# Performance work log

Hardware: AMD Instinct MI355X
Metric: run time of the kernel (lower is better)

The kernel has to match this reference:

```python
import jax, jax.numpy as jnp
import numpy as np

SEQ, BATCH, HID = 4096, 32, 512


def setup_inputs() -> dict:
    key = jax.random.key(0)
    ks = jax.random.split(key, 7)
    s = 1.0 / np.sqrt(HID)
    return {
        "x0": jax.random.normal(ks[0], (SEQ, BATCH, 1), dtype=jnp.float32),
        "W_ih": jax.random.uniform(ks[1], (4 * HID, 1), jnp.float32, -s, s),
        "W_hh": jax.random.uniform(ks[2], (4 * HID, HID), jnp.float32, -s, s),
        "b_ih": jax.random.uniform(ks[3], (4 * HID,), jnp.float32, -s, s),
        "b_hh": jax.random.uniform(ks[4], (4 * HID,), jnp.float32, -s, s),
        "W_lin": jax.random.uniform(ks[5], (1, HID), jnp.float32, -s, s),
        "b_lin": jax.random.uniform(ks[6], (1,), jnp.float32, -s, s),
    }


def _lstm(x0, W_ih, W_hh, b_ih, b_hh):
    # x0: (T, B, 1). Precompute input contribution to gates for all steps.
    x_proj = jnp.einsum("tbi,gi->tbg", x0, W_ih) + (b_ih + b_hh)  # (T, B, 4H)
    T, B, _ = x_proj.shape
    H = W_hh.shape[1]
    h0 = jnp.zeros((B, H), x0.dtype)
    c0 = jnp.zeros((B, H), x0.dtype)

    def step(carry, xp):
        h, c = carry
        gates = xp + h @ W_hh.T  # (B, 4H)
        i, f, g, o = jnp.split(gates, 4, axis=-1)  # torch gate order i,f,g,o
        i = jax.nn.sigmoid(i)
        f = jax.nn.sigmoid(f)
        g = jnp.tanh(g)
        o = jax.nn.sigmoid(o)
        c = f * c + i * g
        h = o * jnp.tanh(c)
        return (h, c), h

    _, hs = jax.lax.scan(step, (h0, c0), x_proj)  # hs: (T, B, H)
    return hs


def reference(x0, W_ih, W_hh, b_ih, b_hh, W_lin, b_lin):
    hs = _lstm(x0, W_ih, W_hh, b_ih, b_hh)            # (T, B, H)
    y = jnp.einsum("tbh,oh->tbo", hs, W_lin) + b_lin  # (T, B, 1)
    return y + x0                                      # residual add
```

## Files before the change

### kernel.cpp

```cpp
#include <hip/hip_runtime.h>
#include <stdint.h>

#define T_STEPS 4096
#define BATCH 32
#define HID 512
#define GROUPS 8
#define BLK_THREADS 512
#define NBLOCKS 256
#define SLOT_DW (BATCH * GROUPS * 64)

typedef _Float16 h2_t __attribute__((ext_vector_type(2)));
typedef uint32_t u32x8 __attribute__((ext_vector_type(8)));

__device__ inline uint32_t pack_h2(float a, float b) {
  h2_t v;
  v.x = (_Float16)a;
  v.y = (_Float16)b;
  return __builtin_bit_cast(uint32_t, v);
}

__device__ inline float fdot2(uint32_t a, uint32_t b, float c) {
  return __builtin_amdgcn_fdot2(__builtin_bit_cast(h2_t, a),
                                __builtin_bit_cast(h2_t, b), c, false);
}

__device__ inline uint64_t uni64(const void* p) {
  uint32_t lo = __builtin_amdgcn_readfirstlane((uint32_t)(uintptr_t)p);
  uint32_t hi = __builtin_amdgcn_readfirstlane((uint32_t)((uintptr_t)p >> 32));
  return ((uint64_t)hi << 32) | lo;
}

__device__ inline void kinv() {
  asm volatile("s_dcache_inv" ::: "memory");
}

__device__ inline void sload_rec(uint64_t p, u32x8* d0, u32x8* d1,
                                 u32x8* d2, u32x8* d3,
                                 uint32_t* t0, uint32_t* t1,
                                 uint32_t* t2, uint32_t* t3) {
  asm volatile("s_load_dwordx8 %0, %8, 0x0\n\t"
               "s_load_dword %4, %8, 0x20\n\t"
               "s_load_dwordx8 %1, %8, 0x40\n\t"
               "s_load_dword %5, %8, 0x60\n\t"
               "s_load_dwordx8 %2, %8, 0x80\n\t"
               "s_load_dword %6, %8, 0xa0\n\t"
               "s_load_dwordx8 %3, %8, 0xc0\n\t"
               "s_load_dword %7, %8, 0xe0\n\t"
               "s_waitcnt lgkmcnt(0)"
               : "=&s"(*d0), "=&s"(*d1), "=&s"(*d2), "=&s"(*d3),
                 "=&s"(*t0), "=&s"(*t1), "=&s"(*t2), "=&s"(*t3)
               : "s"(p) : "memory");
}

__device__ inline float sigf(float x) { return 1.0f / (1.0f + __expf(-x)); }
__device__ inline float tanh_fast(float x) {
  float a = fabsf(x);
  float e = __expf(-2.0f * a);
  float r = (1.0f - e) / (1.0f + e);
  return copysignf(r, x);
}

__global__ __launch_bounds__(BLK_THREADS)
void lstm_w8(const float* __restrict__ x0,
             const float* __restrict__ W_ih,
             const float* __restrict__ W_hh,
             const float* __restrict__ b_ih,
             const float* __restrict__ b_hh,
             const float* __restrict__ W_lin,
             const float* __restrict__ b_lin,
             float* __restrict__ y,
             uint32_t* __restrict__ h_ex,
             int* __restrict__ claim)
{
  __shared__ float x0_lds[T_STEPS];
  __shared__ float ylds[T_STEPS];
  __shared__ float gacc[2][256];
  __shared__ int arrive[2];
  __shared__ int s_bg;

  const int tid = threadIdx.x;

  if (tid == 0) {
    uint32_t xcc;
    asm volatile("s_getreg_b32 %0, hwreg(HW_REG_XCC_ID)" : "=s"(xcc));
    xcc &= 7;
    int slot = atomicAdd(claim + xcc * 16, 1);
    s_bg = (slot < 32) ? (int)(((4 * xcc + (slot >> 3)) << 3) | (slot & 7))
                       : -1;
  }
  __syncthreads();
  if (s_bg < 0) return;
  const int b  = s_bg >> 3;
  const int g  = s_bg & 7;
  const int u0 = g * 64;
  const int wv = tid >> 6;
  const int cs = wv;
  const int l  = tid & 63;

  uint32_t w[4][32];
#pragma unroll
  for (int a = 0; a < 4; ++a) {
    const int R = a * HID + u0 + l;
    const float2* p = (const float2*)(W_hh + (size_t)R * HID + 64 * cs);
#pragma unroll
    for (int k = 0; k < 32; ++k) {
      float2 q = p[k];
      w[a][k] = pack_h2(q.x, q.y);
    }
  }
  for (int i = tid; i < T_STEPS; i += BLK_THREADS) {
    x0_lds[i] = x0[i * BATCH + b];
    ylds[i] = 0.f;
  }
  if (tid < 256) { gacc[0][tid] = 0.f; gacc[1][tid] = 0.f; }
  if (tid < 2) arrive[tid] = 0;

  float c_state = 0.f;
  float wih_[4] = {0.f, 0.f, 0.f, 0.f}, bs_[4] = {0.f, 0.f, 0.f, 0.f};
  float wlin_u = 0.f, blin = 0.f;
  if (tid < 64) {
#pragma unroll
    for (int j = 0; j < 4; ++j) {
      int R = j * HID + u0 + tid;
      wih_[j] = W_ih[R];
      bs_[j] = b_ih[R] + b_hh[R];
    }
    wlin_u = W_lin[u0 + tid];
    blin = b_lin[0];
  }

  uint32_t* hb = h_ex + (size_t)b * (GROUPS * 64);
  const uint64_t dpu[2] = { uni64(hb + 64 * cs),
                            uni64(hb + SLOT_DW + 64 * cs) };
  uint32_t* pub01[2] = { hb + 64 * g, hb + SLOT_DW + 64 * g };

  __syncthreads();

  int dead = 0;
  for (int t = 0; t < T_STEPS; ++t) {
    const int sl = t & 1, ns = sl ^ 1;

    u32x8 D0, D1, D2, D3;
    uint32_t tg0, tg1, tg2, tg3;
    {
      const uint32_t want = (uint32_t)t;
      int guard = 0;
      for (;;) {
        kinv();
        sload_rec(dpu[sl], &D0, &D1, &D2, &D3, &tg0, &tg1, &tg2, &tg3);
        if ((tg0 == want) & (tg1 == want) &
            (tg2 == want) & (tg3 == want)) break;
        if (dead || ++guard > (1 << 14)) { dead = 1; break; }
      }
    }

    __builtin_amdgcn_s_setprio(1);
    float ae0 = 0.f, ao0 = 0.f, ae1 = 0.f, ao1 = 0.f;
    float ae2 = 0.f, ao2 = 0.f, ae3 = 0.f, ao3 = 0.f;
#pragma unroll
    for (int k = 0; k < 8; k += 2) {
      ae0 = fdot2(w[0][k], D0[k], ae0);      ao0 = fdot2(w[0][k + 1], D0[k + 1], ao0);
      ae1 = fdot2(w[1][k], D0[k], ae1);      ao1 = fdot2(w[1][k + 1], D0[k + 1], ao1);
      ae2 = fdot2(w[2][k], D0[k], ae2);      ao2 = fdot2(w[2][k + 1], D0[k + 1], ao2);
      ae3 = fdot2(w[3][k], D0[k], ae3);      ao3 = fdot2(w[3][k + 1], D0[k + 1], ao3);
      ae0 = fdot2(w[0][8 + k], D1[k], ae0);  ao0 = fdot2(w[0][9 + k], D1[k + 1], ao0);
      ae1 = fdot2(w[1][8 + k], D1[k], ae1);  ao1 = fdot2(w[1][9 + k], D1[k + 1], ao1);
      ae2 = fdot2(w[2][8 + k], D1[k], ae2);  ao2 = fdot2(w[2][9 + k], D1[k + 1], ao2);
      ae3 = fdot2(w[3][8 + k], D1[k], ae3);  ao3 = fdot2(w[3][9 + k], D1[k + 1], ao3);
      ae0 = fdot2(w[0][16 + k], D2[k], ae0); ao0 = fdot2(w[0][17 + k], D2[k + 1], ao0);
      ae1 = fdot2(w[1][16 + k], D2[k], ae1); ao1 = fdot2(w[1][17 + k], D2[k + 1], ao1);
      ae2 = fdot2(w[2][16 + k], D2[k], ae2); ao2 = fdot2(w[2][17 + k], D2[k + 1], ao2);
      ae3 = fdot2(w[3][16 + k], D2[k], ae3); ao3 = fdot2(w[3][17 + k], D2[k + 1], ao3);
      ae0 = fdot2(w[0][24 + k], D3[k], ae0); ao0 = fdot2(w[0][25 + k], D3[k + 1], ao0);
      ae1 = fdot2(w[1][24 + k], D3[k], ae1); ao1 = fdot2(w[1][25 + k], D3[k + 1], ao1);
      ae2 = fdot2(w[2][24 + k], D3[k], ae2); ao2 = fdot2(w[2][25 + k], D3[k + 1], ao2);
      ae3 = fdot2(w[3][24 + k], D3[k], ae3); ao3 = fdot2(w[3][25 + k], D3[k + 1], ao3);
    }
    atomicAdd(&gacc[sl][l],       ae0 + ao0);
    atomicAdd(&gacc[sl][64 + l],  ae1 + ao1);
    atomicAdd(&gacc[sl][128 + l], ae2 + ao2);
    atomicAdd(&gacc[sl][192 + l], ae3 + ao3);
    asm volatile("" ::: "memory");
    if (l == 0) atomicAdd(&arrive[sl], 1);
    __builtin_amdgcn_s_setprio(0);

    if (tid < 64) {
      {
        int guard = 0;
        while (((volatile int*)arrive)[sl] < 8) {
          if (++guard > (1 << 20)) break;
        }
      }
      asm volatile("" ::: "memory");
      __builtin_amdgcn_s_setprio(1);
      arrive[sl] = 0;

      const float xv = x0_lds[t];
      float gi = gacc[sl][tid]       + xv * wih_[0] + bs_[0];
      float gf = gacc[sl][tid + 64]  + xv * wih_[1] + bs_[1];
      float gg = gacc[sl][tid + 128] + xv * wih_[2] + bs_[2];
      float go = gacc[sl][tid + 192] + xv * wih_[3] + bs_[3];
      float si = sigf(gi), sf = sigf(gf), tg_ = tanh_fast(gg), so = sigf(go);
      c_state = sf * c_state + si * tg_;
      float h = so * tanh_fast(c_state);

      float hn = __shfl_down(h, 1, 64);
      uint32_t val = 0;
      int doff = 0;
      bool act = false;
      if ((tid & 1) == 0) {
        int j = tid >> 1;
        val = pack_h2(h, hn);
        doff = ((j >> 3) << 4) + (j & 7);
        act = true;
      } else if (tid < 8) {
        int L = (tid - 1) >> 1;
        val = (uint32_t)(t + 1);
        doff = (L << 4) + 8;
        act = true;
      }
      if (act) pub01[ns][doff] = val;

      gacc[sl][tid] = 0.f;
      gacc[sl][tid + 64] = 0.f;
      gacc[sl][tid + 128] = 0.f;
      gacc[sl][tid + 192] = 0.f;

      float p = wlin_u * h;
#pragma unroll
      for (int m = 32; m >= 1; m >>= 1) p += __shfl_xor(p, m, 64);
      if (tid == 0) ylds[t] = p;
      __builtin_amdgcn_s_setprio(0);
    }
  }

  __syncthreads();
  for (int i = tid; i < T_STEPS; i += BLK_THREADS) {
    float val = ylds[i];
    if (g == 0) val += blin + x0_lds[i];
    unsafeAtomicAdd(&y[i * BATCH + b], val);
  }
}

extern "C" void kernel_launch(void* const* d_in, const int* in_sizes, int n_in,
                              void* d_out, int out_size, void* d_ws, size_t ws_size,
                              hipStream_t stream) {
  const float* x0    = (const float*)d_in[0];
  const float* W_ih  = (const float*)d_in[1];
  const float* W_hh  = (const float*)d_in[2];
  const float* b_ih  = (const float*)d_in[3];
  const float* b_hh  = (const float*)d_in[4];
  const float* W_lin = (const float*)d_in[5];
  const float* b_lin = (const float*)d_in[6];
  float* y = (float*)d_out;

  uint32_t* h_ex = (uint32_t*)d_ws;
  int* claim     = (int*)(h_ex + 2 * SLOT_DW);
  const size_t init_bytes = (size_t)2 * SLOT_DW * sizeof(uint32_t)
                            + 8 * 16 * sizeof(int);

  (void)hipMemsetAsync(d_ws, 0, init_bytes, stream);
  (void)hipMemsetAsync(d_out, 0, (size_t)out_size * sizeof(float), stream);

  hipLaunchKernelGGL(lstm_w8, dim3(NBLOCKS), dim3(BLK_THREADS), 0, stream,
                     x0, W_ih, W_hh, b_ih, b_hh, W_lin, b_lin, y, h_ex, claim);
}
```

Baseline: 13.97 ms.

## Let wave 0 consume its own hidden slice from LDS and skip global polling

Each block's wave 0 now handles the column slice that this block produces itself (cs rotated by the group index). It reads that slice from a small LDS ring buffer instead of polling global memory, so the wave no longer waits on a global round trip for its own data. Wave 0 also takes over the gate nonlinearity, and the output projection for the previous step is deferred and computed from the fp16-rounded h stored in LDS. This moves work off the critical path between steps. The cost is that y is now computed from fp16-rounded h, which adds a small precision loss, and wave 0 carries more work per step.

```diff
diff --git a/kernel.cpp b/kernel.cpp
--- a/kernel.cpp
+++ b/kernel.cpp
@@ -10,6 +10,7 @@
 #define SLOT_DW (BATCH * GROUPS * 64)
 
 typedef _Float16 h2_t __attribute__((ext_vector_type(2)));
+typedef uint32_t u32x4 __attribute__((ext_vector_type(4)));
 typedef uint32_t u32x8 __attribute__((ext_vector_type(8)));
 
 __device__ inline uint32_t pack_h2(float a, float b) {
@@ -61,20 +62,21 @@
 }
 
 __global__ __launch_bounds__(BLK_THREADS)
-void lstm_w8(const float* __restrict__ x0,
-             const float* __restrict__ W_ih,
-             const float* __restrict__ W_hh,
-             const float* __restrict__ b_ih,
-             const float* __restrict__ b_hh,
-             const float* __restrict__ W_lin,
-             const float* __restrict__ b_lin,
-             float* __restrict__ y,
-             uint32_t* __restrict__ h_ex,
-             int* __restrict__ claim)
+void lstm_w8t(const float* __restrict__ x0,
+              const float* __restrict__ W_ih,
+              const float* __restrict__ W_hh,
+              const float* __restrict__ b_ih,
+              const float* __restrict__ b_hh,
+              const float* __restrict__ W_lin,
+              const float* __restrict__ b_lin,
+              float* __restrict__ y,
+              uint32_t* __restrict__ h_ex,
+              int* __restrict__ claim)
 {
   __shared__ float x0_lds[T_STEPS];
   __shared__ float ylds[T_STEPS];
   __shared__ float gacc[2][256];
+  __shared__ __align__(16) uint32_t h_self[4][32];
   __shared__ int arrive[2];
   __shared__ int s_bg;
 
@@ -94,7 +96,7 @@
   const int g  = s_bg & 7;
   const int u0 = g * 64;
   const int wv = tid >> 6;
-  const int cs = wv;
+  const int cs = (g + wv) & 7;
   const int l  = tid & 63;
 
   uint32_t w[4][32];
@@ -113,11 +115,13 @@
     ylds[i] = 0.f;
   }
   if (tid < 256) { gacc[0][tid] = 0.f; gacc[1][tid] = 0.f; }
+  if (tid < 128) ((uint32_t*)h_self)[tid] = 0;
   if (tid < 2) arrive[tid] = 0;
 
   float c_state = 0.f;
   float wih_[4] = {0.f, 0.f, 0.f, 0.f}, bs_[4] = {0.f, 0.f, 0.f, 0.f};
-  float wlin_u = 0.f, blin = 0.f;
+  float wlin_u = 0.f;
+  const float blin = b_lin[0];
   if (tid < 64) {
 #pragma unroll
     for (int j = 0; j < 4; ++j) {
@@ -126,7 +130,6 @@
       bs_[j] = b_ih[R] + b_hh[R];
     }
     wlin_u = W_lin[u0 + tid];
-    blin = b_lin[0];
   }
 
   uint32_t* hb = h_ex + (size_t)b * (GROUPS * 64);
@@ -140,98 +143,136 @@
   for (int t = 0; t < T_STEPS; ++t) {
     const int sl = t & 1, ns = sl ^ 1;
 
-    u32x8 D0, D1, D2, D3;
-    uint32_t tg0, tg1, tg2, tg3;
+    if (wv != 0) {
+      u32x8 D0, D1, D2, D3;
+      uint32_t tg0, tg1, tg2, tg3;
+      {
+        const uint32_t want = (uint32_t)t;
+        int guard = 0;
+        for (;;) {
+          kinv();
+          sload_rec(dpu[sl], &D0, &D1, &D2, &D3, &tg0, &tg1, &tg2, &tg3);
+          if ((tg0 == want) & (tg1 == want) &
+              (tg2 == want) & (tg3 == want)) break;
+          if (dead || ++guard > (1 << 14)) { dead = 1; break; }
+        }
+      }
+      __builtin_amdgcn_s_setprio(1);
+      float ae0 = 0.f, ao0 = 0.f, ae1 = 0.f, ao1 = 0.f;
+      float ae2 = 0.f, ao2 = 0.f, ae3 = 0.f, ao3 = 0.f;
+#pragma unroll
+      for (int k = 0; k < 8; k += 2) {
+        ae0 = fdot2(w[0][k], D0[k], ae0);      ao0 = fdot2(w[0][k + 1], D0[k + 1], ao0);
+        ae1 = fdot2(w[1][k], D0[k], ae1);      ao1 = fdot2(w[1][k + 1], D0[k + 1], ao1);
+        ae2 = fdot2(w[2][k], D0[k], ae2);      ao2 = fdot2(w[2][k + 1], D0[k + 1], ao2);
+        ae3 = fdot2(w[3][k], D0[k], ae3);      ao3 = fdot2(w[3][k + 1], D0[k + 1], ao3);
+        ae0 = fdot2(w[0][8 + k], D1[k], ae0);  ao0 = fdot2(w[0][9 + k], D1[k + 1], ao0);
+        ae1 = fdot2(w[1][8 + k], D1[k], ae1);  ao1 = fdot2(w[1][9 + k], D1[k + 1], ao1);
+        ae2 = fdot2(w[2][8 + k], D1[k], ae2);  ao2 = fdot2(w[2][9 + k], D1[k + 1], ao2);
+        ae3 = fdot2(w[3][8 + k], D1[k], ae3);  ao3 = fdot2(w[3][9 + k], D1[k + 1], ao3);
+        ae0 = fdot2(w[0][16 + k], D2[k], ae0); ao0 = fdot2(w[0][17 + k], D2[k + 1], ao0);
+        ae1 = fdot2(w[1][16 + k], D2[k], ae1); ao1 = fdot2(w[1][17 + k], D2[k + 1], ao1);
+        ae2 = fdot2(w[2][16 + k], D2[k], ae2); ao2 = fdot2(w[2][17 + k], D2[k + 1], ao2);
+        ae3 = fdot2(w[3][16 + k], D2[k], ae3); ao3 = fdot2(w[3][17 + k], D2[k + 1], ao3);
+        ae0 = fdot2(w[0][24 + k], D3[k], ae0); ao0 = fdot2(w[0][25 + k], D3[k + 1], ao0);
+        ae1 = fdot2(w[1][24 + k], D3[k], ae1); ao1 = fdot2(w[1][25 + k], D3[k + 1], ao1);
+        ae2 = fdot2(w[2][24 + k], D3[k], ae2); ao2 = fdot2(w[2][25 + k], D3[k + 1], ao2);
+        ae3 = fdot2(w[3][24 + k], D3[k], ae3); ao3 = fdot2(w[3][25 + k], D3[k + 1], ao3);
+      }
+      atomicAdd(&gacc[sl][l],       ae0 + ao0);
+      atomicAdd(&gacc[sl][64 + l],  ae1 + ao1);
+      atomicAdd(&gacc[sl][128 + l], ae2 + ao2);
+      atomicAdd(&gacc[sl][192 + l], ae3 + ao3);
+      asm volatile("" ::: "memory");
+      if (l == 0) atomicAdd(&arrive[sl], 1);
+      __builtin_amdgcn_s_setprio(0);
+      continue;
+    }
+
+    __builtin_amdgcn_s_setprio(1);
     {
-      const uint32_t want = (uint32_t)t;
+      const u32x4* Vb = (const u32x4*)h_self[t & 3];
+      float ae0 = 0.f, ao0 = 0.f, ae1 = 0.f, ao1 = 0.f;
+      float ae2 = 0.f, ao2 = 0.f, ae3 = 0.f, ao3 = 0.f;
+#pragma unroll
+      for (int q = 0; q < 8; ++q) {
+        u32x4 V = Vb[q];
+#pragma unroll
+        for (int j = 0; j < 4; j += 2) {
+          const int k = 4 * q + j;
+          ae0 = fdot2(w[0][k], V[j], ae0);  ao0 = fdot2(w[0][k + 1], V[j + 1], ao0);
+          ae1 = fdot2(w[1][k], V[j], ae1);  ao1 = fdot2(w[1][k + 1], V[j + 1], ao1);
+          ae2 = fdot2(w[2][k], V[j], ae2);  ao2 = fdot2(w[2][k + 1], V[j + 1], ao2);
+          ae3 = fdot2(w[3][k], V[j], ae3);  ao3 = fdot2(w[3][k + 1], V[j + 1], ao3);
+        }
+      }
+      atomicAdd(&gacc[sl][l],       ae0 + ao0);
+      atomicAdd(&gacc[sl][64 + l],  ae1 + ao1);
+      atomicAdd(&gacc[sl][128 + l], ae2 + ao2);
+      atomicAdd(&gacc[sl][192 + l], ae3 + ao3);
+      asm volatile("" ::: "memory");
+      if (l == 0) atomicAdd(&arrive[sl], 1);
+    }
+
+    if (t > 0) {
+      uint16_t hu = ((volatile uint16_t*)h_self[t & 3])[l];
+      float p = wlin_u * (float)__builtin_bit_cast(_Float16, hu);
+#pragma unroll
+      for (int m = 32; m >= 1; m >>= 1) p += __shfl_xor(p, m, 64);
+      if (l == 0) ylds[t - 1] = p;
+    }
+
+    {
       int guard = 0;
-      for (;;) {
-        kinv();
-        sload_rec(dpu[sl], &D0, &D1, &D2, &D3, &tg0, &tg1, &tg2, &tg3);
-        if ((tg0 == want) & (tg1 == want) &
-            (tg2 == want) & (tg3 == want)) break;
-        if (dead || ++guard > (1 << 14)) { dead = 1; break; }
-      }
-    }
-
-    __builtin_amdgcn_s_setprio(1);
-    float ae0 = 0.f, ao0 = 0.f, ae1 = 0.f, ao1 = 0.f;
-    float ae2 = 0.f, ao2 = 0.f, ae3 = 0.f, ao3 = 0.f;
-#pragma unroll
-    for (int k = 0; k < 8; k += 2) {
-      ae0 = fdot2(w[0][k], D0[k], ae0);      ao0 = fdot2(w[0][k + 1], D0[k + 1], ao0);
-      ae1 = fdot2(w[1][k], D0[k], ae1);      ao1 = fdot2(w[1][k + 1], D0[k + 1], ao1);
-      ae2 = fdot2(w[2][k], D0[k], ae2);      ao2 = fdot2(w[2][k + 1], D0[k + 1], ao2);
-      ae3 = fdot2(w[3][k], D0[k], ae3);      ao3 = fdot2(w[3][k + 1], D0[k + 1], ao3);
-      ae0 = fdot2(w[0][8 + k], D1[k], ae0);  ao0 = fdot2(w[0][9 + k], D1[k + 1], ao0);
-      ae1 = fdot2(w[1][8 + k], D1[k], ae1);  ao1 = fdot2(w[1][9 + k], D1[k + 1], ao1);
-      ae2 = fdot2(w[2][8 + k], D1[k], ae2);  ao2 = fdot2(w[2][9 + k], D1[k + 1], ao2);
-      ae3 = fdot2(w[3][8 + k], D1[k], ae3);  ao3 = fdot2(w[3][9 + k], D1[k + 1], ao3);
-      ae0 = fdot2(w[0][16 + k], D2[k], ae0); ao0 = fdot2(w[0][17 + k], D2[k + 1], ao0);
-      ae1 = fdot2(w[1][16 + k], D2[k], ae1); ao1 = fdot2(w[1][17 + k], D2[k + 1], ao1);
-      ae2 = fdot2(w[2][16 + k], D2[k], ae2); ao2 = fdot2(w[2][17 + k], D2[k + 1], ao2);
-      ae3 = fdot2(w[3][16 + k], D2[k], ae3); ao3 = fdot2(w[3][17 + k], D2[k + 1], ao3);
-      ae0 = fdot2(w[0][24 + k], D3[k], ae0); ao0 = fdot2(w[0][25 + k], D3[k + 1], ao0);
-      ae1 = fdot2(w[1][24 + k], D3[k], ae1); ao1 = fdot2(w[1][25 + k], D3[k + 1], ao1);
-      ae2 = fdot2(w[2][24 + k], D3[k], ae2); ao2 = fdot2(w[2][25 + k], D3[k + 1], ao2);
-      ae3 = fdot2(w[3][24 + k], D3[k], ae3); ao3 = fdot2(w[3][25 + k], D3[k + 1], ao3);
-    }
-    atomicAdd(&gacc[sl][l],       ae0 + ao0);
-    atomicAdd(&gacc[sl][64 + l],  ae1 + ao1);
-    atomicAdd(&gacc[sl][128 + l], ae2 + ao2);
-    atomicAdd(&gacc[sl][192 + l], ae3 + ao3);
+      while (((volatile int*)arrive)[sl] < 8) {
+        if (++guard > (1 << 20)) break;
+      }
+    }
     asm volatile("" ::: "memory");
-    if (l == 0) atomicAdd(&arrive[sl], 1);
-    __builtin_amdgcn_s_setprio(0);
-
-    if (tid < 64) {
-      {
-        int guard = 0;
-        while (((volatile int*)arrive)[sl] < 8) {
-          if (++guard > (1 << 20)) break;
-        }
-      }
-      asm volatile("" ::: "memory");
-      __builtin_amdgcn_s_setprio(1);
-      arrive[sl] = 0;
-
-      const float xv = x0_lds[t];
-      float gi = gacc[sl][tid]       + xv * wih_[0] + bs_[0];
-      float gf = gacc[sl][tid + 64]  + xv * wih_[1] + bs_[1];
-      float gg = gacc[sl][tid + 128] + xv * wih_[2] + bs_[2];
-      float go = gacc[sl][tid + 192] + xv * wih_[3] + bs_[3];
-      float si = sigf(gi), sf = sigf(gf), tg_ = tanh_fast(gg), so = sigf(go);
-      c_state = sf * c_state + si * tg_;
-      float h = so * tanh_fast(c_state);
-
-      float hn = __shfl_down(h, 1, 64);
+    arrive[sl] = 0;
+
+    const float xv = x0_lds[t];
+    float gi = gacc[sl][l]       + xv * wih_[0] + bs_[0];
+    float gf = gacc[sl][l + 64]  + xv * wih_[1] + bs_[1];
+    float gg = gacc[sl][l + 128] + xv * wih_[2] + bs_[2];
+    float go = gacc[sl][l + 192] + xv * wih_[3] + bs_[3];
+    float si = sigf(gi), sf = sigf(gf), tg_ = tanh_fast(gg), so = sigf(go);
+    c_state = sf * c_state + si * tg_;
+    float h = so * tanh_fast(c_state);
+
+    float hn = __shfl_down(h, 1, 64);
+    uint32_t pk = pack_h2(h, hn);
+    {
       uint32_t val = 0;
       int doff = 0;
       bool act = false;
-      if ((tid & 1) == 0) {
-        int j = tid >> 1;
-        val = pack_h2(h, hn);
+      if ((l & 1) == 0) {
+        int j = l >> 1;
+        val = pk;
         doff = ((j >> 3) << 4) + (j & 7);
         act = true;
-      } else if (tid < 8) {
-        int L = (tid - 1) >> 1;
+      } else if (l < 8) {
+        int L = (l - 1) >> 1;
         val = (uint32_t)(t + 1);
         doff = (L << 4) + 8;
         act = true;
       }
       if (act) pub01[ns][doff] = val;
-
-      gacc[sl][tid] = 0.f;
-      gacc[sl][tid + 64] = 0.f;
-      gacc[sl][tid + 128] = 0.f;
-      gacc[sl][tid + 192] = 0.f;
-
-      float p = wlin_u * h;
-#pragma unroll
-      for (int m = 32; m >= 1; m >>= 1) p += __shfl_xor(p, m, 64);
-      if (tid == 0) ylds[t] = p;
-      __builtin_amdgcn_s_setprio(0);
-    }
+    }
+    if ((l & 1) == 0) h_self[(t + 1) & 3][l >> 1] = pk;
+    gacc[sl][l] = 0.f;
+    gacc[sl][l + 64] = 0.f;
+    gacc[sl][l + 128] = 0.f;
+    gacc[sl][l + 192] = 0.f;
+    __builtin_amdgcn_s_setprio(0);
+  }
+
+  if (wv == 0) {
+    uint16_t hu = ((volatile uint16_t*)h_self[T_STEPS & 3])[l];
+    float p = wlin_u * (float)__builtin_bit_cast(_Float16, hu);
+#pragma unroll
+    for (int m = 32; m >= 1; m >>= 1) p += __shfl_xor(p, m, 64);
+    if (l == 0) ylds[T_STEPS - 1] = p;
   }
 
   __syncthreads();
@@ -262,6 +303,6 @@
   (void)hipMemsetAsync(d_ws, 0, init_bytes, stream);
   (void)hipMemsetAsync(d_out, 0, (size_t)out_size * sizeof(float), stream);
 
-  hipLaunchKernelGGL(lstm_w8, dim3(NBLOCKS), dim3(BLK_THREADS), 0, stream,
+  hipLaunchKernelGGL(lstm_w8t, dim3(NBLOCKS), dim3(BLK_THREADS), 0, stream,
                      x0, W_ih, W_hh, b_ih, b_hh, W_lin, b_lin, y, h_ex, claim);
 }
```

New measurement: 14.47 ms. +3.6%, slower.
